# Optimization experiments

Hardware: AMD Instinct MI355X
Metric: run time of the kernel (lower is better)

## Reference

```python
import jax, jax.numpy as jnp
import numpy as np

H, DR, DN = 16, 64, 64
HD = DR + DN  # 128
EPS = 1e-6


def _ln(t):
    m = t.mean(-1, keepdims=True)
    v = ((t - m) ** 2).mean(-1, keepdims=True)
    return (t - m) / jnp.sqrt(v + EPS)


def _rms(t, w):
    return t * jax.lax.rsqrt((t * t).mean(-1, keepdims=True) + EPS) * w


def _rot(t, fcs):
    # t: [b,s,h,DR]; fcs: [s, DR//2, 2] (cos,sin); complex multiply on pairs
    b, s, h, d = t.shape
    tr = t.reshape(b, s, h, d // 2, 2)
    x0, x1 = tr[..., 0], tr[..., 1]
    cos = fcs[None, :, None, :, 0]
    sin = fcs[None, :, None, :, 1]
    o0 = x0 * cos - x1 * sin
    o1 = x0 * sin + x1 * cos
    return jnp.stack([o0, o1], axis=-1).reshape(b, s, h, d)


def setup_inputs() -> dict:
    key = jax.random.key(0)
    ks = jax.random.split(key, 12)
    B, SX, SY, D = 1, 2048, 512, 2048
    s = 0.02
    pos_x = jnp.arange(SX, dtype=jnp.float32)
    pos_y = jnp.arange(SY, dtype=jnp.float32)
    inv = 1.0 / (10000.0 ** (jnp.arange(0, DR, 2, dtype=jnp.float32) / DR))  # [32]
    ang_x = pos_x[:, None] * inv[None, :]
    ang_y = pos_y[:, None] * inv[None, :]
    return {
        "x": jax.random.normal(ks[0], (B, SX, D), jnp.float32),
        "y": jax.random.normal(ks[1], (B, SY, D), jnp.float32),
        "mod": jax.random.normal(ks[2], (B, D), jnp.float32),
        "freqs_x": jnp.stack([jnp.cos(ang_x), jnp.sin(ang_x)], -1),
        "freqs_y": jnp.stack([jnp.cos(ang_y), jnp.sin(ang_y)], -1),
        "mask_x": jnp.ones((B, SX), bool),
        "mask_y": jnp.ones((B, SY), bool),
        "Wqkv_x": jax.random.normal(ks[3], (HD * H * 3, D), jnp.float32) * s,
        "bqkv_x": jnp.zeros((HD * H * 3,), jnp.float32),
        "Wqkv_y": jax.random.normal(ks[4], (HD * H * 3, D), jnp.float32) * s,
        "bqkv_y": jnp.zeros((HD * H * 3,), jnp.float32),
        "Wout": jax.random.normal(ks[5], (D, HD * H), jnp.float32) * s,
        "bout": jnp.zeros((D,), jnp.float32),
        "wq": jnp.ones((HD,), jnp.float32),
        "wk": jnp.ones((HD,), jnp.float32),
        "Wmod_q": jax.random.normal(ks[6], (D * 3, D), jnp.float32) * s,
        "bmod_q": jnp.zeros((D * 3,), jnp.float32),
        "Wmod_kv": jax.random.normal(ks[7], (D * 3, D), jnp.float32) * s,
        "bmod_kv": jnp.zeros((D * 3,), jnp.float32),
    }


def reference(x, y, mod, freqs_x, freqs_y, mask_x, mask_y, Wqkv_x, bqkv_x,
              Wqkv_y, bqkv_y, Wout, bout, wq, wk, Wmod_q, bmod_q, Wmod_kv, bmod_kv):
    b, sx, D = x.shape
    sy = y.shape[1]
    sz = sx + sy
    x_res, y_res = x, y
    xn = _ln(x)
    yn = _ln(y)
    # modulation from mod vector [b, D] -> [b, 1, 3D]
    mq = mod[:, None, :] @ Wmod_q.T + bmod_q
    bias_x, scale_x, gate_x = jnp.split(mq, 3, axis=-1)
    mkv = mod[:, None, :] @ Wmod_kv.T + bmod_kv
    bias_y, scale_y, gate_y = jnp.split(mkv, 3, axis=-1)
    xm = (1.0 + scale_x) * xn + bias_x
    ym = (1.0 + scale_y) * yn + bias_y
    qx, kx, vx = jnp.split(xm @ Wqkv_x.T + bqkv_x, 3, axis=-1)
    qy, ky, vy = jnp.split(ym @ Wqkv_y.T + bqkv_y, 3, axis=-1)
    q = jnp.concatenate([qx, qy], 1).reshape(b, sz, H, HD)
    k = jnp.concatenate([kx, ky], 1).reshape(b, sz, H, HD)
    v = jnp.concatenate([vx, vy], 1).reshape(b, sz, H, HD)
    q = _rms(q, wq)
    k = _rms(k, wk)
    q_rope, q_nope = q[..., :DR], q[..., DR:]
    k_rope, k_nope = k[..., :DR], k[..., DR:]
    fxx = jnp.concatenate([freqs_x, jnp.zeros_like(freqs_y)], 0)
    fyy = jnp.concatenate([jnp.zeros_like(freqs_x), freqs_y], 0)
    qf = jnp.concatenate([_rot(q_rope, fxx), _rot(q_rope, fyy), q_nope], -1)
    kf = jnp.concatenate([_rot(k_rope, fxx), _rot(k_rope, fyy), k_nope], -1)
    d_attn = 2 * DR + DN  # 192
    scale = 1.0 / jnp.sqrt(jnp.float32(d_attn))
    scores = jnp.einsum('bshd,bthd->bhst', qf, kf) * scale
    mask = jnp.concatenate([mask_x, mask_y], 1)  # [b, sz] bool, key-side
    scores = jnp.where(mask[:, None, None, :], scores, -jnp.inf)
    attn = jax.nn.softmax(scores, axis=-1)
    z = jnp.einsum('bhst,bthd->bshd', attn, v).reshape(b, sz, H * HD)
    z = z @ Wout.T + bout
    xo = z[:, :sx] * gate_x + x_res
    yo = z[:, sx:] * gate_y + y_res
    return jnp.concatenate([xo, yo], axis=1)  # [b, sz, D]
```

## Files before the change

kernel.cpp:

```cpp
#include <hip/hip_runtime.h>
#include <math.h>

#define H_    16
#define DR_   64
#define HD_   128
#define D_    2048
#define SX_   2048
#define SY_   512
#define SZ_   2560
#define NQKV_ 6144
#define EPS_  1e-6f
#define ATTN_SCALE 0.07216878364870323f
#define NS_   4
#define SPL_  (SZ_ / NS_)
#define QT_   (SZ_ / 128)

typedef __attribute__((ext_vector_type(8)))  short short8;
typedef __attribute__((ext_vector_type(16))) float f32x16;

__device__ __forceinline__ unsigned short f2bf(float f) {
    unsigned u = __builtin_bit_cast(unsigned, f);
    u += 0x7FFF + ((u >> 16) & 1);
    return (unsigned short)(u >> 16);
}
__device__ __forceinline__ unsigned pack2(float a, float b) {
    return (unsigned)f2bf(a) | ((unsigned)f2bf(b) << 16);
}
__device__ __forceinline__ float bf2f_lo(unsigned u) {
    return __builtin_bit_cast(float, u << 16);
}
__device__ __forceinline__ float bf2f_hi(unsigned u) {
    return __builtin_bit_cast(float, u & 0xffff0000u);
}

__device__ __forceinline__ unsigned cvtpk_bf16(float lo, float hi) {
    unsigned r;
    asm volatile("v_cvt_pk_bf16_f32 %0, %1, %2" : "=v"(r) : "v"(lo), "v"(hi));
    return r;
}

__device__ __forceinline__ void gload16(const unsigned short* g, unsigned short* l) {
    __builtin_amdgcn_global_load_lds(
        (const __attribute__((address_space(1))) unsigned*)g,
        (__attribute__((address_space(3))) unsigned*)l, 16, 0, 0);
}

__device__ __forceinline__ short8 mkfrag(const float* p) {
    unsigned a01 = cvtpk_bf16(p[0], p[1]);
    unsigned a23 = cvtpk_bf16(p[2], p[3]);
    unsigned a45 = cvtpk_bf16(p[4], p[5]);
    unsigned a67 = cvtpk_bf16(p[6], p[7]);
    asm volatile("v_permlane32_swap_b32 %0, %1" : "+v"(a01), "+v"(a45));
    asm volatile("v_permlane32_swap_b32 %0, %1" : "+v"(a23), "+v"(a67));
    union { unsigned u[4]; short8 s; } r;
    r.u[0] = a01; r.u[1] = a23; r.u[2] = a45; r.u[3] = a67;
    return r.s;
}

__global__ __launch_bounds__(256) void cvt_bf16_kernel(
    const float* __restrict__ src, unsigned short* __restrict__ dst, int n)
{
    int i = (blockIdx.x * 256 + threadIdx.x) * 8;
    if (i >= n) return;
    float4 a = *(const float4*)(src + i);
    float4 b = *(const float4*)(src + i + 4);
    uint4 pk;
    pk.x = pack2(a.x, a.y); pk.y = pack2(a.z, a.w);
    pk.z = pack2(b.x, b.y); pk.w = pack2(b.z, b.w);
    *(uint4*)(dst + i) = pk;
}

__global__ __launch_bounds__(256) void mod_gemv_kernel(
    const float* __restrict__ mod,
    const float* __restrict__ Wq, const float* __restrict__ bq,
    const float* __restrict__ Wkv, const float* __restrict__ bkv,
    float* __restrict__ mq, float* __restrict__ mkv)
{
    int t = threadIdx.x;
    int row = blockIdx.x * 4 + (t >> 6);
    int lane = t & 63;
    const float* W; const float* b; float* out; int r;
    if (row < NQKV_) { W = Wq;  b = bq;  out = mq;  r = row; }
    else             { W = Wkv; b = bkv; out = mkv; r = row - NQKV_; }
    const float* wr = W + (size_t)r * D_;
    float s = 0.f;
    for (int k = lane; k < D_; k += 64) s += wr[k] * mod[k];
#pragma unroll
    for (int m = 32; m >= 1; m >>= 1) s += __shfl_xor(s, m);
    if (lane == 0) out[r] = s + b[r];
}

__global__ __launch_bounds__(256) void ln_mod_kernel(
    const float* __restrict__ x, const float* __restrict__ y,
    const float* __restrict__ mq, const float* __restrict__ mkv,
    unsigned short* __restrict__ xm)
{
    __shared__ float red[8];
    int s = blockIdx.x, t = threadIdx.x;
    const float* src; const float* mv;
    if (s < SX_) { src = x + (size_t)s * D_;          mv = mq; }
    else         { src = y + (size_t)(s - SX_) * D_;  mv = mkv; }
    float a[8];
    *(float4*)&a[0] = *(const float4*)(src + t * 8);
    *(float4*)&a[4] = *(const float4*)(src + t * 8 + 4);
    float sum = 0.f, ssq = 0.f;
#pragma unroll
    for (int i = 0; i < 8; ++i) { sum += a[i]; ssq += a[i] * a[i]; }
#pragma unroll
    for (int m = 32; m >= 1; m >>= 1) { sum += __shfl_xor(sum, m); ssq += __shfl_xor(ssq, m); }
    if ((t & 63) == 0) { red[t >> 6] = sum; red[4 + (t >> 6)] = ssq; }
    __syncthreads();
    float tot  = red[0] + red[1] + red[2] + red[3];
    float totq = red[4] + red[5] + red[6] + red[7];
    float mean = tot * (1.f / (float)D_);
    float var  = totq * (1.f / (float)D_) - mean * mean;
    float inv  = rsqrtf(var + EPS_);
    float o[8];
#pragma unroll
    for (int i = 0; i < 8; ++i) {
        int c = t * 8 + i;
        float v = (a[i] - mean) * inv;
        o[i] = (1.f + mv[D_ + c]) * v + mv[c];
    }
    uint4 pk;
    pk.x = pack2(o[0], o[1]); pk.y = pack2(o[2], o[3]);
    pk.z = pack2(o[4], o[5]); pk.w = pack2(o[6], o[7]);
    *(uint4*)(xm + (size_t)s * D_ + t * 8) = pk;
}

__global__ __launch_bounds__(256) void gemm_bf16_kernel(
    const unsigned short* __restrict__ A,
    const unsigned short* __restrict__ Wx, const float* __restrict__ bx,
    const unsigned short* __restrict__ Wy, const float* __restrict__ by,
    void* __restrict__ Cout, int N,
    const float* __restrict__ gx, const float* __restrict__ gy,
    const float* __restrict__ rx, const float* __restrict__ ry,
    int mode)
{
    __shared__ __align__(16) unsigned short As[128 * 32];
    __shared__ __align__(16) unsigned short Bs[128 * 32];
    int m0 = blockIdx.y * 128, n0 = blockIdx.x * 128;
    const unsigned short* W = (m0 < SX_) ? Wx : Wy;
    const float* bb = (m0 < SX_) ? bx : by;
    int t = threadIdx.x;
    int wv = t >> 6, lane = t & 63, l31 = lane & 31, g = lane >> 5;
    int wr = wv >> 1, wc = wv & 1;
    int srow = t >> 2, ssl = t & 3;
    const unsigned short* gA = A + (size_t)(m0 + srow) * D_ + ((ssl ^ (srow & 3)) * 8);
    const unsigned short* gW = W + (size_t)(n0 + srow) * D_ + ((ssl ^ (srow & 3)) * 8);
    f32x16 acc[2][2];
#pragma unroll
    for (int i = 0; i < 2; ++i)
#pragma unroll
        for (int j = 0; j < 2; ++j)
#pragma unroll
            for (int r = 0; r < 16; ++r) acc[i][j][r] = 0.f;
    int arow = wr * 64 + l31;
    int wrow = wc * 64 + l31;
    int a3 = arow & 3, w3 = wrow & 3;

    for (int k0 = 0; k0 < D_; k0 += 32) {
        __syncthreads();
        gload16(gA + k0,            &As[wv * 512]);
        gload16(gA + 64 * D_ + k0,  &As[2048 + wv * 512]);
        gload16(gW + k0,            &Bs[wv * 512]);
        gload16(gW + 64 * D_ + k0,  &Bs[2048 + wv * 512]);
        __syncthreads();
#pragma unroll
        for (int kk = 0; kk < 2; ++kk) {
            int slot = kk * 2 + g;
            short8 af[2], wf[2];
#pragma unroll
            for (int i = 0; i < 2; ++i) {
                af[i] = *(const short8*)&As[(arow + i * 32) * 32 + ((slot ^ a3) * 8)];
                wf[i] = *(const short8*)&Bs[(wrow + i * 32) * 32 + ((slot ^ w3) * 8)];
            }
#pragma unroll
            for (int i = 0; i < 2; ++i)
#pragma unroll
                for (int j = 0; j < 2; ++j)
                    acc[i][j] = __builtin_amdgcn_mfma_f32_32x32x16_bf16(wf[j], af[i], acc[i][j], 0, 0, 0);
        }
    }

#pragma unroll
    for (int i = 0; i < 2; ++i) {
        int row = m0 + wr * 64 + i * 32 + l31;
        if (mode == 0) {
            unsigned short* C = (unsigned short*)Cout;
#pragma unroll
            for (int j = 0; j < 2; ++j)
#pragma unroll
                for (int q = 0; q < 4; ++q) {
                    int n = n0 + wc * 64 + j * 32 + q * 8 + 4 * g;
                    float o0 = acc[i][j][q * 4 + 0] + bb[n + 0];
                    float o1 = acc[i][j][q * 4 + 1] + bb[n + 1];
                    float o2 = acc[i][j][q * 4 + 2] + bb[n + 2];
                    float o3 = acc[i][j][q * 4 + 3] + bb[n + 3];
                    *(uint2*)(C + (size_t)row * N + n) = make_uint2(pack2(o0, o1), pack2(o2, o3));
                }
        } else {
            float* C = (float*)Cout;
            const float* gt = (row < SX_) ? gx : gy;
            const float* rr = (row < SX_) ? rx + (size_t)row * N : ry + (size_t)(row - SX_) * N;
#pragma unroll
            for (int j = 0; j < 2; ++j)
#pragma unroll
                for (int q = 0; q < 4; ++q) {
                    int n = n0 + wc * 64 + j * 32 + q * 8 + 4 * g;
                    float4 o;
                    o.x = (acc[i][j][q * 4 + 0] + bb[n + 0]) * gt[n + 0] + rr[n + 0];
                    o.y = (acc[i][j][q * 4 + 1] + bb[n + 1]) * gt[n + 1] + rr[n + 1];
                    o.z = (acc[i][j][q * 4 + 2] + bb[n + 2]) * gt[n + 2] + rr[n + 2];
                    o.w = (acc[i][j][q * 4 + 3] + bb[n + 3]) * gt[n + 3] + rr[n + 3];
                    *(float4*)(C + (size_t)row * N + n) = o;
                }
        }
    }
}

__global__ __launch_bounds__(256) void qkv_transform_kernel(
    const unsigned short* __restrict__ qkv,
    const float* __restrict__ fx, const float* __restrict__ fy,
    const float* __restrict__ wq, const float* __restrict__ wk,
    unsigned short* __restrict__ qh, unsigned short* __restrict__ kh,
    unsigned short* __restrict__ vh)
{
    int t = threadIdx.x;
    int gid = blockIdx.x * 4 + (t >> 6);
    int lane = t & 63;
    int s = gid >> 4;
    int h = gid & 15;
    const unsigned short* base = qkv + (size_t)s * NQKV_ + h * HD_;
    int d = lane * 2;
    unsigned qu = *(const unsigned*)(base + d);
    unsigned ku = *(const unsigned*)(base + 2048 + d);
    unsigned vu = *(const unsigned*)(base + 4096 + d);
    float qx = bf2f_lo(qu), qy = bf2f_hi(qu);
    float kx = bf2f_lo(ku), ky = bf2f_hi(ku);
    float sq = qx * qx + qy * qy;
    float sk = kx * kx + ky * ky;
#pragma unroll
    for (int m = 32; m >= 1; m >>= 1) { sq += __shfl_xor(sq, m); sk += __shfl_xor(sk, m); }
    float qs = rsqrtf(sq * (1.f / 128.f) + EPS_) * ATTN_SCALE;
    float ks = rsqrtf(sk * (1.f / 128.f) + EPS_);
    float q0 = qx * qs * wq[d], q1 = qy * qs * wq[d + 1];
    float k0 = kx * ks * wk[d], k1 = ky * ks * wk[d + 1];
    if (lane < 32) {
        const float* f = (s < SX_) ? fx + (size_t)s * DR_ + d
                                   : fy + (size_t)(s - SX_) * DR_ + d;
        float cs = f[0], sn = f[1];
        float o0 = q0 * cs - q1 * sn, o1 = q0 * sn + q1 * cs;
        q0 = o0; q1 = o1;
        o0 = k0 * cs - k1 * sn; o1 = k0 * sn + k1 * cs;
        k0 = o0; k1 = o1;
    }
    size_t off = ((size_t)h * SZ_ + s) * HD_ + d;
    *(unsigned*)(qh + off) = pack2(q0, q1);
    *(unsigned*)(kh + off) = pack2(k0, k1);
    *(unsigned*)(vh + off) = vu;
}

__global__ __launch_bounds__(256) void vtrans_kernel(
    const unsigned short* __restrict__ vh, unsigned short* __restrict__ vt)
{
    __shared__ __align__(16) unsigned short T[64][72];
    int h = blockIdx.z, d0 = blockIdx.y * 64, s0 = blockIdx.x * 64;
    int t = threadIdx.x;
    int r = t >> 2, c = (t & 3) * 16;
    const unsigned short* src = vh + ((size_t)h * SZ_ + s0 + r) * HD_ + d0 + c;
    *(short8*)&T[r][c]     = *(const short8*)(src);
    *(short8*)&T[r][c + 8] = *(const short8*)(src + 8);
    __syncthreads();
    unsigned short o16[16];
#pragma unroll
    for (int i = 0; i < 16; ++i) o16[i] = T[c + i][r];
    unsigned short* dst = vt + ((size_t)h * HD_ + d0 + r) * SZ_ + s0 + c;
    *(short8*)dst       = *(short8*)&o16[0];
    *(short8*)(dst + 8) = *(short8*)&o16[8];
}

__global__ __launch_bounds__(256) void attn_mfma_kernel(
    const unsigned short* __restrict__ qh, const unsigned short* __restrict__ kh,
    const unsigned short* __restrict__ vt,
    unsigned short* __restrict__ Opart, float* __restrict__ mpart, float* __restrict__ lpart)
{
    __shared__ __align__(16) short Ks[2][64 * 128];
    __shared__ __align__(16) short Vs[2][128 * 64];
    int h = blockIdx.y;
    int split = blockIdx.z;
    int t = threadIdx.x;
    int wv = t >> 6, lane = t & 63;
    int l31 = lane & 31, g = lane >> 5;
    int bq = blockIdx.x * 128 + wv * 32;
    const unsigned short* kbase = kh + (size_t)h * SZ_ * HD_;
    const unsigned short* vbase = vt + (size_t)h * HD_ * SZ_;

    int koff[4], voff[4];
#pragma unroll
    for (int i = 0; i < 4; ++i) {
        int idx = i * 256 + t;
        int r = idx >> 4, sl = idx & 15;
        koff[i] = r * HD_ + (((sl & 8) | ((sl ^ (r & 7)) & 7)) * 8);
        int r2 = idx >> 3, sl2 = idx & 7;
        voff[i] = r2 * SZ_ + ((sl2 ^ (r2 & 7)) * 8);
    }
    int ldsOff = wv * 512;

    short8 qf[8];
    {
        const unsigned short* qb = qh + ((size_t)h * SZ_ + bq + l31) * HD_ + g * 8;
#pragma unroll
        for (int s = 0; s < 8; ++s) qf[s] = *(const short8*)(qb + s * 16);
    }

    f32x16 o[4];
#pragma unroll
    for (int db = 0; db < 4; ++db)
#pragma unroll
        for (int r = 0; r < 16; ++r) o[db][r] = 0.f;
    float mreg = -INFINITY, lreg = 0.f;
    bool qY = (bq >= SX_);
    int sw7 = l31 & 7;
    int ts0 = split * SPL_;
    const int NT = SPL_ / 64;

#pragma unroll
    for (int i = 0; i < 4; ++i)
        gload16(kbase + (size_t)ts0 * HD_ + koff[i], (unsigned short*)&Ks[0][0] + i * 2048 + ldsOff);
#pragma unroll
    for (int i = 0; i < 4; ++i)
        gload16(vbase + ts0 + voff[i], (unsigned short*)&Vs[0][0] + i * 2048 + ldsOff);
    __syncthreads();

    for (int it = 0; it < NT; ++it) {
        int t0 = ts0 + it * 64;
        int cur = it & 1;
        if (it + 1 < NT) {
            int nb = cur ^ 1;
            const unsigned short* kn = kbase + (size_t)(t0 + 64) * HD_;
            const unsigned short* vn = vbase + (t0 + 64);
#pragma unroll
            for (int i = 0; i < 4; ++i)
                gload16(kn + koff[i], (unsigned short*)&Ks[nb][0] + i * 2048 + ldsOff);
#pragma unroll
            for (int i = 0; i < 4; ++i)
                gload16(vn + voff[i], (unsigned short*)&Vs[nb][0] + i * 2048 + ldsOff);
        }

        bool same = (qY == (t0 >= SX_));
        f32x16 sc0, sc1;
#pragma unroll
        for (int r = 0; r < 16; ++r) { sc0[r] = 0.f; sc1[r] = 0.f; }
        const short* Krow0 = &Ks[cur][0] + l31 * 128;
        const short* Krow1 = &Ks[cur][0] + (l31 + 32) * 128;
        __builtin_amdgcn_s_setprio(1);
#pragma unroll
        for (int s = 4; s < 8; ++s) {
            int slot = 2 * s + g;
            int sl = (slot & 8) | ((slot ^ sw7) & 7);
            sc0 = __builtin_amdgcn_mfma_f32_32x32x16_bf16(*(const short8*)(Krow0 + sl * 8), qf[s], sc0, 0, 0, 0);
            sc1 = __builtin_amdgcn_mfma_f32_32x32x16_bf16(*(const short8*)(Krow1 + sl * 8), qf[s], sc1, 0, 0, 0);
        }
        if (same) {
#pragma unroll
            for (int s = 0; s < 4; ++s) {
                int slot = 2 * s + g;
                int sl = (slot & 8) | ((slot ^ sw7) & 7);
                sc0 = __builtin_amdgcn_mfma_f32_32x32x16_bf16(*(const short8*)(Krow0 + sl * 8), qf[s], sc0, 0, 0, 0);
                sc1 = __builtin_amdgcn_mfma_f32_32x32x16_bf16(*(const short8*)(Krow1 + sl * 8), qf[s], sc1, 0, 0, 0);
            }
        }
        __builtin_amdgcn_s_setprio(0);

        float pm = -INFINITY;
#pragma unroll
        for (int r = 0; r < 16; ++r) pm = fmaxf(pm, fmaxf(sc0[r], sc1[r]));
        pm = fmaxf(pm, __shfl_xor(pm, 32));
        float mnew = fmaxf(mreg, pm);
        float corr = __expf(mreg - mnew);
        mreg = mnew;
        float pp0[16], pp1[16]; float rs = 0.f;
#pragma unroll
        for (int r = 0; r < 16; ++r) {
            pp0[r] = __expf(sc0[r] - mnew);
            pp1[r] = __expf(sc1[r] - mnew);
            rs += pp0[r] + pp1[r];
        }
        rs += __shfl_xor(rs, 32);
        lreg = lreg * corr + rs;
#pragma unroll
        for (int db = 0; db < 4; ++db)
#pragma unroll
            for (int r = 0; r < 16; ++r) o[db][r] *= corr;

        short8 pa0 = mkfrag(&pp0[0]), pa1 = mkfrag(&pp0[8]);
        short8 pa2 = mkfrag(&pp1[0]), pa3 = mkfrag(&pp1[8]);
        const short* Vb = &Vs[cur][0];
        __builtin_amdgcn_s_setprio(1);
#pragma unroll
        for (int ks = 0; ks < 4; ++ks) {
            short8 pf = (ks == 0) ? pa0 : (ks == 1) ? pa1 : (ks == 2) ? pa2 : pa3;
#pragma unroll
            for (int db = 0; db < 4; ++db) {
                int row = db * 32 + l31;
                int sl = (2 * ks + g) ^ (l31 & 7);
                const short8 vf = *(const short8*)(Vb + row * 64 + sl * 8);
                o[db] = __builtin_amdgcn_mfma_f32_32x32x16_bf16(vf, pf, o[db], 0, 0, 0);
            }
        }
        __builtin_amdgcn_s_setprio(0);
        __syncthreads();
    }

    int basep = ((split * QT_ + blockIdx.x) * H_ + h) * 128 + wv * 32 + l31;
    unsigned short* op = Opart + (size_t)basep * 128;
#pragma unroll
    for (int db = 0; db < 4; ++db)
#pragma unroll
        for (int r = 0; r < 16; ++r) {
            int d = db * 32 + (r & 3) + 8 * (r >> 2) + 4 * g;
            op[d] = f2bf(o[db][r]);
        }
    if (g == 0) { mpart[basep] = mreg; lpart[basep] = lreg; }
}

__global__ __launch_bounds__(256) void attn_combine_kernel(
    const unsigned short* __restrict__ Opart,
    const float* __restrict__ mpart, const float* __restrict__ lpart,
    unsigned short* __restrict__ z)
{
    int t = threadIdx.x;
    int gid = blockIdx.x * 4 + (t >> 6);
    int lane = t & 63;
    int h = gid & 15;
    int r = gid >> 4;
    int qtile = r >> 7, qi = r & 127;
    int pidx[NS_];
    float m[NS_];
    float mx = -INFINITY;
#pragma unroll
    for (int s = 0; s < NS_; ++s) {
        pidx[s] = ((s * QT_ + qtile) * H_ + h) * 128 + qi;
        m[s] = mpart[pidx[s]];
        mx = fmaxf(mx, m[s]);
    }
    float L = 0.f;
    float w[NS_];
#pragma unroll
    for (int s = 0; s < NS_; ++s) {
        w[s] = __expf(m[s] - mx);
        L += w[s] * lpart[pidx[s]];
    }
    float invL = 1.f / L;
    int d = lane * 2;
    float a0 = 0.f, a1 = 0.f;
#pragma unroll
    for (int s = 0; s < NS_; ++s) {
        unsigned u = *(const unsigned*)(Opart + (size_t)pidx[s] * 128 + d);
        a0 += w[s] * bf2f_lo(u);
        a1 += w[s] * bf2f_hi(u);
    }
    *(unsigned*)(z + (size_t)r * D_ + h * HD_ + d) = pack2(a0 * invL, a1 * invL);
}

extern "C" void kernel_launch(void* const* d_in, const int* in_sizes, int n_in,
                              void* d_out, int out_size, void* d_ws, size_t ws_size,
                              hipStream_t stream) {
    const float* x    = (const float*)d_in[0];
    const float* y    = (const float*)d_in[1];
    const float* mod  = (const float*)d_in[2];
    const float* fx   = (const float*)d_in[3];
    const float* fy   = (const float*)d_in[4];
    const float* Wqx  = (const float*)d_in[7];
    const float* bqx  = (const float*)d_in[8];
    const float* Wqy  = (const float*)d_in[9];
    const float* bqy  = (const float*)d_in[10];
    const float* Wout = (const float*)d_in[11];
    const float* bout = (const float*)d_in[12];
    const float* wq   = (const float*)d_in[13];
    const float* wk   = (const float*)d_in[14];
    const float* Wmq  = (const float*)d_in[15];
    const float* bmq  = (const float*)d_in[16];
    const float* Wmk  = (const float*)d_in[17];
    const float* bmk  = (const float*)d_in[18];

    float* mq   = (float*)d_ws;
    float* mkv  = mq + NQKV_;
    unsigned short* xm   = (unsigned short*)(mkv + NQKV_);
    unsigned short* qkvb = xm + (size_t)SZ_ * D_;
    unsigned short* qh   = qkvb + (size_t)SZ_ * NQKV_;
    unsigned short* kh   = qh + (size_t)H_ * SZ_ * HD_;
    unsigned short* vh   = kh + (size_t)H_ * SZ_ * HD_;
    unsigned short* vt   = vh + (size_t)H_ * SZ_ * HD_;
    unsigned short* wqxb = vt + (size_t)H_ * SZ_ * HD_;
    unsigned short* wqyb = wqxb + (size_t)NQKV_ * D_;
    unsigned short* wob  = wqyb + (size_t)NQKV_ * D_;
    unsigned short* z    = xm;
    unsigned short* Opart = wqxb;
    float* mpart = (float*)qkvb;
    float* lpart = mpart + NS_ * QT_ * H_ * 128;
    float* out  = (float*)d_out;

    hipLaunchKernelGGL(cvt_bf16_kernel, dim3(NQKV_ * D_ / 2048), dim3(256), 0, stream,
                       Wqx, wqxb, NQKV_ * D_);
    hipLaunchKernelGGL(cvt_bf16_kernel, dim3(NQKV_ * D_ / 2048), dim3(256), 0, stream,
                       Wqy, wqyb, NQKV_ * D_);
    hipLaunchKernelGGL(cvt_bf16_kernel, dim3(D_ * D_ / 2048), dim3(256), 0, stream,
                       Wout, wob, D_ * D_);
    hipLaunchKernelGGL(mod_gemv_kernel, dim3(2 * NQKV_ / 4), dim3(256), 0, stream,
                       mod, Wmq, bmq, Wmk, bmk, mq, mkv);
    hipLaunchKernelGGL(ln_mod_kernel, dim3(SZ_), dim3(256), 0, stream,
                       x, y, mq, mkv, xm);
    hipLaunchKernelGGL(gemm_bf16_kernel, dim3(NQKV_ / 128, SZ_ / 128), dim3(256), 0, stream,
                       xm, wqxb, bqx, wqyb, bqy, (void*)qkvb, NQKV_,
                       (const float*)nullptr, (const float*)nullptr,
                       (const float*)nullptr, (const float*)nullptr, 0);
    hipLaunchKernelGGL(qkv_transform_kernel, dim3(SZ_ * H_ / 4), dim3(256), 0, stream,
                       qkvb, fx, fy, wq, wk, qh, kh, vh);
    hipLaunchKernelGGL(vtrans_kernel, dim3(SZ_ / 64, HD_ / 64, H_), dim3(256), 0, stream,
                       vh, vt);
    hipLaunchKernelGGL(attn_mfma_kernel, dim3(QT_, H_, NS_), dim3(256), 0, stream,
                       qh, kh, vt, Opart, mpart, lpart);
    hipLaunchKernelGGL(attn_combine_kernel, dim3(SZ_ * H_ / 4), dim3(256), 0, stream,
                       Opart, mpart, lpart, z);
    hipLaunchKernelGGL(gemm_bf16_kernel, dim3(D_ / 128, SZ_ / 128), dim3(256), 0, stream,
                       z, wob, bout, wob, bout, (void*)out, D_,
                       mq + 2 * D_, mkv + 2 * D_, x, y, 1);
}
```

Measured before the change: 357.7 us.

## Double-buffer GEMM shared-memory tiles and change the LDS swizzle pattern

The bf16 GEMM now keeps two shared-memory buffers for the A and B tiles. It issues the global-to-LDS loads for the next K slice before running the MFMAs on the current one, and needs one barrier per iteration instead of two. The XOR swizzle key moves from row&3 to (row>>1)&3 to reduce LDS bank conflicts on the fragment reads. LDS use per block doubles, which may lower occupancy. Correctness depends on gload16 completing before the barrier, since there is no explicit wait on the async load.

```diff
diff --git a/kernel.cpp b/kernel.cpp
--- a/kernel.cpp
+++ b/kernel.cpp
@@ -137,8 +137,8 @@
     const float* __restrict__ rx, const float* __restrict__ ry,
     int mode)
 {
-    __shared__ __align__(16) unsigned short As[128 * 32];
-    __shared__ __align__(16) unsigned short Bs[128 * 32];
+    __shared__ __align__(16) unsigned short As[2][128 * 32];
+    __shared__ __align__(16) unsigned short Bs[2][128 * 32];
     int m0 = blockIdx.y * 128, n0 = blockIdx.x * 128;
     const unsigned short* W = (m0 < SX_) ? Wx : Wy;
     const float* bb = (m0 < SX_) ? bx : by;
@@ -146,8 +146,8 @@
     int wv = t >> 6, lane = t & 63, l31 = lane & 31, g = lane >> 5;
     int wr = wv >> 1, wc = wv & 1;
     int srow = t >> 2, ssl = t & 3;
-    const unsigned short* gA = A + (size_t)(m0 + srow) * D_ + ((ssl ^ (srow & 3)) * 8);
-    const unsigned short* gW = W + (size_t)(n0 + srow) * D_ + ((ssl ^ (srow & 3)) * 8);
+    const unsigned short* gA = A + (size_t)(m0 + srow) * D_ + ((ssl ^ ((srow >> 1) & 3)) * 8);
+    const unsigned short* gW = W + (size_t)(n0 + srow) * D_ + ((ssl ^ ((srow >> 1) & 3)) * 8);
     f32x16 acc[2][2];
 #pragma unroll
     for (int i = 0; i < 2; ++i)
@@ -157,23 +157,31 @@
             for (int r = 0; r < 16; ++r) acc[i][j][r] = 0.f;
     int arow = wr * 64 + l31;
     int wrow = wc * 64 + l31;
-    int a3 = arow & 3, w3 = wrow & 3;
+    int a3 = (arow >> 1) & 3, w3 = (wrow >> 1) & 3;
+
+    gload16(gA,            &As[0][wv * 512]);
+    gload16(gA + 64 * D_,  &As[0][2048 + wv * 512]);
+    gload16(gW,            &Bs[0][wv * 512]);
+    gload16(gW + 64 * D_,  &Bs[0][2048 + wv * 512]);
+    __syncthreads();
 
     for (int k0 = 0; k0 < D_; k0 += 32) {
-        __syncthreads();
-        gload16(gA + k0,            &As[wv * 512]);
-        gload16(gA + 64 * D_ + k0,  &As[2048 + wv * 512]);
-        gload16(gW + k0,            &Bs[wv * 512]);
-        gload16(gW + 64 * D_ + k0,  &Bs[2048 + wv * 512]);
-        __syncthreads();
+        int cur = (k0 >> 5) & 1;
+        if (k0 + 32 < D_) {
+            int nb = cur ^ 1;
+            gload16(gA + k0 + 32,           &As[nb][wv * 512]);
+            gload16(gA + 64 * D_ + k0 + 32, &As[nb][2048 + wv * 512]);
+            gload16(gW + k0 + 32,           &Bs[nb][wv * 512]);
+            gload16(gW + 64 * D_ + k0 + 32, &Bs[nb][2048 + wv * 512]);
+        }
 #pragma unroll
         for (int kk = 0; kk < 2; ++kk) {
             int slot = kk * 2 + g;
             short8 af[2], wf[2];
 #pragma unroll
             for (int i = 0; i < 2; ++i) {
-                af[i] = *(const short8*)&As[(arow + i * 32) * 32 + ((slot ^ a3) * 8)];
-                wf[i] = *(const short8*)&Bs[(wrow + i * 32) * 32 + ((slot ^ w3) * 8)];
+                af[i] = *(const short8*)&As[cur][(arow + i * 32) * 32 + ((slot ^ a3) * 8)];
+                wf[i] = *(const short8*)&Bs[cur][(wrow + i * 32) * 32 + ((slot ^ w3) * 8)];
             }
 #pragma unroll
             for (int i = 0; i < 2; ++i)
@@ -181,6 +189,7 @@
                 for (int j = 0; j < 2; ++j)
                     acc[i][j] = __builtin_amdgcn_mfma_f32_32x32x16_bf16(wf[j], af[i], acc[i][j], 0, 0, 0);
         }
+        __syncthreads();
     }
 
 #pragma unroll
```

Measured after the change: 360.3 us. Within noise of the previous version (+0.7%).
